# Kernel tuning notes

Hardware: AMD Instinct MI355X
Metric: run time of the kernel (lower is better)

Reference implementation:

```python
import jax, jax.numpy as jnp
import numpy as np


def setup_inputs() -> dict:
    key = jax.random.key(0)
    k1, k2, k3, k4 = jax.random.split(key, 4)
    N, Cin, H, W = 4, 32, 64, 64
    Cout, K = 64, 3
    fan = Cin * K * K
    x = jax.random.normal(k1, (N, Cin, H, W), jnp.float32)
    # kaiming_normal init for AEG weight; standard conv init for the dense conv
    weight = jax.random.normal(k2, (Cout, Cin, K, K), jnp.float32) * np.float32(np.sqrt(2.0 / fan))
    conv_w = jax.random.normal(k3, (Cout, Cin, K, K), jnp.float32) * np.float32(np.sqrt(1.0 / fan))
    conv_b = jax.random.normal(k4, (Cout,), jnp.float32) * np.float32(0.01)
    return {"x": x, "weight": weight, "conv_w": conv_w, "conv_b": conv_b}


def _aeg_conv(x, weight, stride, padding):
    # Faithful translation of conv2d_aeg_optimized, but the per-tap recurrence
    # runs under lax.scan and never materializes the (N,Cout,Cin,K2,L) tensor.
    N, Cin, H, W = x.shape
    Cout, _, KH, KW = weight.shape
    xp = jnp.pad(x, ((0, 0), (0, 0), (padding, padding), (padding, padding)))
    oh = (H - KH + 2 * padding) // stride + 1
    ow = (W - KW + 2 * padding) // stride + 1
    # per-tap shifted views of the padded input: (K2, N, Cin, oh, ow)
    taps = jnp.stack([
        xp[:, :, ki:ki + (oh - 1) * stride + 1:stride, kj:kj + (ow - 1) * stride + 1:stride]
        for ki in range(KH) for kj in range(KW)
    ])
    kflat = weight.reshape(Cout, Cin, KH * KW).transpose(2, 0, 1)  # (K2, Cout, Cin)
    # mask[k, i, j] = (i + j + k) % 2 == 0 where i = l // ow, j = l % ow
    ii = jnp.arange(oh)[:, None]
    jj = jnp.arange(ow)[None, :]
    kk = jnp.arange(KH * KW)[:, None, None]
    mask = (ii + jj + kk) % 2 == 0  # (K2, oh, ow)

    def step(res, tap):
        xk, yk, mk = tap
        xk = xk[:, None]                      # (N, 1, Cin, oh, ow)
        yk = yk[None, :, :, None, None]       # (1, Cout, Cin, 1, 1)
        mk = mk[None, None, None]             # (1, 1, 1, oh, ow)
        res = jnp.where(mk, (res + xk) * yk, (res + yk) * xk)
        return res, None

    res0 = jnp.zeros((N, Cout, Cin, oh, ow), x.dtype)
    res, _ = jax.lax.scan(step, res0, (taps, kflat, mask))
    return res.sum(axis=2)  # (N, Cout, oh, ow)


def reference(x, weight, conv_w, conv_b):
    stride, padding = 1, 1
    aeg = _aeg_conv(x, weight, stride, padding)
    conv = jax.lax.conv_general_dilated(
        x, conv_w, window_strides=(stride, stride),
        padding=[(padding, padding), (padding, padding)],
        dimension_numbers=("NCHW", "OIHW", "NCHW"),
    ) + conv_b[None, :, None, None]
    return jax.nn.sigmoid(aeg) * conv
```

## Files before the change

### kernel.cpp

```cpp
#include <hip/hip_runtime.h>

#define CIN   32
#define COUT  64
#define HH    64
#define WW    64
#define NB    4
#define TH    8
#define HR    (TH + 2)
#define G     8
#define CPT   2
#define ROWCI 72

template<int S>
__device__ __forceinline__ void math_g(const float* __restrict__ sx,
                                       const float* __restrict__ sw,
                                       int lrow, int m, int cb, int g,
                                       float aeg[2][CPT], float cv[2][CPT])
{
    #pragma unroll 2
    for (int cl = 0; cl < G; ++cl) {
        const int ci = g + cl;
        float tc[5], tl[5], tr[5];
        #pragma unroll
        for (int wr = 0; wr < 5; ++wr) {
            const int qc = (wr & 1) ^ 1 ^ S;
            const float* rowp = sx + (lrow + wr) * (G * ROWCI) + cl * ROWCI;
            tc[wr] = rowp[qc * 36 + 1 + m];
            const float* sp = rowp + (1 - qc) * 36 + m + cb;
            tl[wr] = sp[0];
            tr[wr] = sp[1];
        }

        float w[36];
        const float* pw = sw + ci * 36;
        #pragma unroll
        for (int u = 0; u < 9; ++u)
            *(float4*)&w[4 * u] = *(const float4*)&pw[4 * u];

        #pragma unroll
        for (int c = 0; c < CPT; ++c) {
            const float* wA = &w[c * 9];
            const float* wC = &w[18 + c * 9];
            #pragma unroll
            for (int p = 0; p < 2; ++p) {
                float r = 0.0f;
                #pragma unroll
                for (int k = 0; k < 9; ++k) {
                    const int wr = 2 * p + k / 3;
                    const int kj = k % 3;
                    const float t = (kj == 0) ? tl[wr] : ((kj == 1) ? tc[wr] : tr[wr]);
                    const float prod = t * wA[k];
                    r = ((k & 1) == S) ? fmaf(r, wA[k], prod) : fmaf(r, t, prod);
                    cv[p][c] = fmaf(t, wC[k], cv[p][c]);
                }
                aeg[p][c] += r;
            }
        }
    }
}

__global__ __launch_bounds__(256, 4)
void aeg_conv_kernel(const float* __restrict__ x,
                     const float* __restrict__ weight,
                     const float* __restrict__ conv_w,
                     const float* __restrict__ conv_b,
                     float* __restrict__ out)
{
    __shared__ float sx[HR * G * ROWCI];
    __shared__ float sw[CIN * 36];

    const int tid = threadIdx.x;
    const int i0  = blockIdx.x * TH;
    const int n   = blockIdx.y;
    const int co0 = blockIdx.z * CPT;

    const int s  = (tid >> 6) & 1;
    const int rg = tid >> 7;
    const int h  = (tid >> 5) & 1;
    const int m  = tid & 31;

    const int rb_local = rg * 4 + h;
    const int rb  = i0 + rb_local;
    const int cb  = (rb & 1) ^ s;
    const int col = 2 * m + cb;

    const float* xn = x + (size_t)n * (CIN * HH * WW);

    for (int idx = tid; idx < HR * G * 2 * 2; idx += 256) {
        int arr  = idx >> 1;
        int slot = (idx & 1) ? 33 : 0;
        sx[arr * 36 + slot] = 0.0f;
    }

    for (int idx = tid; idx < CIN * 36; idx += 256) {
        int ci = idx / 36, slot = idx - ci * 36;
        int set = slot / 18, rem = slot - set * 18;
        int c2 = rem / 9, k = rem - c2 * 9;
        const float* src = set ? conv_w : weight;
        sw[idx] = src[((size_t)(co0 + c2) * CIN + ci) * 9 + k];
    }

    float aeg[2][CPT], cv[2][CPT];
    #pragma unroll
    for (int p = 0; p < 2; ++p)
        #pragma unroll
        for (int c = 0; c < CPT; ++c) { aeg[p][c] = 0.0f; cv[p][c] = 0.0f; }

    for (int g = 0; g < CIN; g += G) {
        __syncthreads();
        #pragma unroll
        for (int it = 0; it < 5; ++it) {
            int idx  = it * 256 + tid;
            int f4   = idx & 15;
            int pair = idx >> 4;
            int r10  = pair >> 3;
            int cl   = pair & 7;
            int gi   = i0 - 1 + r10;
            float4 v = make_float4(0.f, 0.f, 0.f, 0.f);
            if ((unsigned)gi < (unsigned)HH)
                v = *(const float4*)&xn[(g + cl) * (HH * WW) + gi * WW + 4 * f4];
            int rp   = gi & 1;
            float* base = &sx[pair * ROWCI];
            base[rp * 36 + 1 + 2 * f4]        = v.x;
            base[rp * 36 + 2 + 2 * f4]        = v.z;
            base[(rp ^ 1) * 36 + 1 + 2 * f4]  = v.y;
            base[(rp ^ 1) * 36 + 2 + 2 * f4]  = v.w;
        }
        __syncthreads();

        if (s == 0) math_g<0>(sx, sw, rb_local, m, cb, g, aeg, cv);
        else        math_g<1>(sx, sw, rb_local, m, cb, g, aeg, cv);
    }

    #pragma unroll
    for (int p = 0; p < 2; ++p) {
        int i = rb + 2 * p;
        #pragma unroll
        for (int c = 0; c < CPT; ++c) {
            int co = co0 + c;
            float conv = cv[p][c] + conv_b[co];
            float sg = 1.0f / (1.0f + __expf(-aeg[p][c]));
            out[(((size_t)n * COUT + co) * HH + i) * WW + col] = sg * conv;
        }
    }
}

extern "C" void kernel_launch(void* const* d_in, const int* in_sizes, int n_in,
                              void* d_out, int out_size, void* d_ws, size_t ws_size,
                              hipStream_t stream) {
    const float* x      = (const float*)d_in[0];
    const float* weight = (const float*)d_in[1];
    const float* conv_w = (const float*)d_in[2];
    const float* conv_b = (const float*)d_in[3];
    float* out = (float*)d_out;

    dim3 grid(HH / TH, NB, COUT / CPT);
    aeg_conv_kernel<<<grid, 256, 0, stream>>>(x, weight, conv_w, conv_b, out);
}
```

Before: 37.02 us.

## Pre-pad input into workspace and read conv taps directly from global memory

Adds a separate kernel that writes a zero-padded copy of x (66x68 per channel) into the workspace. The main kernel drops its shared-memory staging of input rows and the per-group barriers, and each thread instead loads unaligned 16-byte float4 rows straight from the padded global buffer, relying on L1/L2 caching for reuse. This removes the LDS traffic and synchronisation, but adds an extra kernel launch and a full read and write of the input, and the float4 loads at odd columns may be misaligned or uncoalesced.

```diff
diff --git a/kernel.cpp b/kernel.cpp
--- a/kernel.cpp
+++ b/kernel.cpp
@@ -6,30 +6,38 @@
 #define WW    64
 #define NB    4
 #define TH    8
-#define HR    (TH + 2)
-#define G     8
 #define CPT   2
-#define ROWCI 72
+#define XPR   66
+#define XPC   68
+
+__global__ __launch_bounds__(256)
+void pad_x(const float* __restrict__ x, float* __restrict__ xp)
+{
+    int idx = blockIdx.x * 256 + threadIdx.x;
+    if (idx >= NB * CIN * XPR * XPC) return;
+    int c  = idx % XPC;
+    int t  = idx / XPC;
+    int r  = t % XPR;
+    int nc = t / XPR;
+    int gi = r - 1, gj = c - 1;
+    float v = 0.0f;
+    if ((unsigned)gi < (unsigned)HH && (unsigned)gj < (unsigned)WW)
+        v = x[(size_t)nc * (HH * WW) + gi * WW + gj];
+    xp[idx] = v;
+}
 
 template<int S>
-__device__ __forceinline__ void math_g(const float* __restrict__ sx,
-                                       const float* __restrict__ sw,
-                                       int lrow, int m, int cb, int g,
-                                       float aeg[2][CPT], float cv[2][CPT])
+__device__ __forceinline__ void math_all(const float* __restrict__ xl,
+                                         const float* __restrict__ sw,
+                                         float aeg[2][CPT], float cv[2][CPT])
 {
-    #pragma unroll 2
-    for (int cl = 0; cl < G; ++cl) {
-        const int ci = g + cl;
-        float tc[5], tl[5], tr[5];
+    #pragma unroll 4
+    for (int ci = 0; ci < CIN; ++ci) {
+        const float* p = xl + ci * (XPR * XPC);
+        float4 t[5];
         #pragma unroll
-        for (int wr = 0; wr < 5; ++wr) {
-            const int qc = (wr & 1) ^ 1 ^ S;
-            const float* rowp = sx + (lrow + wr) * (G * ROWCI) + cl * ROWCI;
-            tc[wr] = rowp[qc * 36 + 1 + m];
-            const float* sp = rowp + (1 - qc) * 36 + m + cb;
-            tl[wr] = sp[0];
-            tr[wr] = sp[1];
-        }
+        for (int wr = 0; wr < 5; ++wr)
+            __builtin_memcpy(&t[wr], p + wr * XPC, 16);
 
         float w[36];
         const float* pw = sw + ci * 36;
@@ -42,31 +50,30 @@
             const float* wA = &w[c * 9];
             const float* wC = &w[18 + c * 9];
             #pragma unroll
-            for (int p = 0; p < 2; ++p) {
+            for (int pp = 0; pp < 2; ++pp) {
                 float r = 0.0f;
                 #pragma unroll
                 for (int k = 0; k < 9; ++k) {
-                    const int wr = 2 * p + k / 3;
+                    const int wr = 2 * pp + k / 3;
                     const int kj = k % 3;
-                    const float t = (kj == 0) ? tl[wr] : ((kj == 1) ? tc[wr] : tr[wr]);
-                    const float prod = t * wA[k];
-                    r = ((k & 1) == S) ? fmaf(r, wA[k], prod) : fmaf(r, t, prod);
-                    cv[p][c] = fmaf(t, wC[k], cv[p][c]);
+                    const float tv = (kj == 0) ? t[wr].x : ((kj == 1) ? t[wr].y : t[wr].z);
+                    const float prod = tv * wA[k];
+                    r = ((k & 1) == S) ? fmaf(r, wA[k], prod) : fmaf(r, tv, prod);
+                    cv[pp][c] = fmaf(tv, wC[k], cv[pp][c]);
                 }
-                aeg[p][c] += r;
+                aeg[pp][c] += r;
             }
         }
     }
 }
 
 __global__ __launch_bounds__(256, 4)
-void aeg_conv_kernel(const float* __restrict__ x,
+void aeg_conv_kernel(const float* __restrict__ xp,
                      const float* __restrict__ weight,
                      const float* __restrict__ conv_w,
                      const float* __restrict__ conv_b,
                      float* __restrict__ out)
 {
-    __shared__ float sx[HR * G * ROWCI];
     __shared__ float sw[CIN * 36];
 
     const int tid = threadIdx.x;
@@ -84,14 +91,6 @@
     const int cb  = (rb & 1) ^ s;
     const int col = 2 * m + cb;
 
-    const float* xn = x + (size_t)n * (CIN * HH * WW);
-
-    for (int idx = tid; idx < HR * G * 2 * 2; idx += 256) {
-        int arr  = idx >> 1;
-        int slot = (idx & 1) ? 33 : 0;
-        sx[arr * 36 + slot] = 0.0f;
-    }
-
     for (int idx = tid; idx < CIN * 36; idx += 256) {
         int ci = idx / 36, slot = idx - ci * 36;
         int set = slot / 18, rem = slot - set * 18;
@@ -99,6 +98,9 @@
         const float* src = set ? conv_w : weight;
         sw[idx] = src[((size_t)(co0 + c2) * CIN + ci) * 9 + k];
     }
+    __syncthreads();
+
+    const float* xl = xp + ((size_t)(n * CIN) * XPR + rb) * XPC + col;
 
     float aeg[2][CPT], cv[2][CPT];
     #pragma unroll
@@ -106,31 +108,8 @@
         #pragma unroll
         for (int c = 0; c < CPT; ++c) { aeg[p][c] = 0.0f; cv[p][c] = 0.0f; }
 
-    for (int g = 0; g < CIN; g += G) {
-        __syncthreads();
-        #pragma unroll
-        for (int it = 0; it < 5; ++it) {
-            int idx  = it * 256 + tid;
-            int f4   = idx & 15;
-            int pair = idx >> 4;
-            int r10  = pair >> 3;
-            int cl   = pair & 7;
-            int gi   = i0 - 1 + r10;
-            float4 v = make_float4(0.f, 0.f, 0.f, 0.f);
-            if ((unsigned)gi < (unsigned)HH)
-                v = *(const float4*)&xn[(g + cl) * (HH * WW) + gi * WW + 4 * f4];
-            int rp   = gi & 1;
-            float* base = &sx[pair * ROWCI];
-            base[rp * 36 + 1 + 2 * f4]        = v.x;
-            base[rp * 36 + 2 + 2 * f4]        = v.z;
-            base[(rp ^ 1) * 36 + 1 + 2 * f4]  = v.y;
-            base[(rp ^ 1) * 36 + 2 + 2 * f4]  = v.w;
-        }
-        __syncthreads();
-
-        if (s == 0) math_g<0>(sx, sw, rb_local, m, cb, g, aeg, cv);
-        else        math_g<1>(sx, sw, rb_local, m, cb, g, aeg, cv);
-    }
+    if (s == 0) math_all<0>(xl, sw, aeg, cv);
+    else        math_all<1>(xl, sw, aeg, cv);
 
     #pragma unroll
     for (int p = 0; p < 2; ++p) {
@@ -153,7 +132,11 @@
     const float* conv_w = (const float*)d_in[2];
     const float* conv_b = (const float*)d_in[3];
     float* out = (float*)d_out;
+    float* xp  = (float*)d_ws;
+
+    const int total = NB * CIN * XPR * XPC;
+    pad_x<<<(total + 255) / 256, 256, 0, stream>>>(x, xp);
 
     dim3 grid(HH / TH, NB, COUT / CPT);
-    aeg_conv_kernel<<<grid, 256, 0, stream>>>(x, weight, conv_w, conv_b, out);
+    aeg_conv_kernel<<<grid, 256, 0, stream>>>(xp, weight, conv_w, conv_b, out);
 }
```

Measured after the change: 50.97 us. 37.7% more time.
